# Optimization experiments

Measured on AMD Instinct MI355X. Metric: run time of the kernel, lower is better.

## Reference

```python
import jax, jax.numpy as jnp
import numpy as np

HIDDEN = 2048
HEADS = 16
HEAD_DIM = HIDDEN // HEADS          # 128
LATENT = HIDDEN // 4                # 512
ROPE_DIM = HEAD_DIM // 2            # 64 (dim passed to LlamaRotaryEmbedding)
B, S = 2, 2048
SCALE = 1.0 / np.sqrt(HEAD_DIM)


def _linear_params(key, d_in, d_out):
    kw, kb = jax.random.split(key)
    bound = 1.0 / np.sqrt(d_in)
    W = jax.random.uniform(kw, (d_in, d_out), jnp.float32, -bound, bound)
    b = jax.random.uniform(kb, (d_out,), jnp.float32, -bound, bound)
    return W, b


def _rope_tables(seq_len):
    # inv_freq over arange(0, ROPE_DIM, 2) -> ROPE_DIM//2 frequencies
    inv_freq = 1.0 / (10000.0 ** (np.arange(0, ROPE_DIM, 2, dtype=np.float32) / ROPE_DIM))
    t = np.arange(seq_len, dtype=np.float32)
    freqs = np.einsum('i,j->ij', t, inv_freq)  # [S, ROPE_DIM//2]
    return jnp.asarray(np.cos(freqs)), jnp.asarray(np.sin(freqs))


def setup_inputs() -> dict:
    key = jax.random.key(0)
    ks = jax.random.split(key, 10)
    x = jax.random.normal(ks[0], (B, S, HIDDEN), jnp.float32)
    # causal mask: 1 where attending allowed, 0 above the diagonal
    attention_mask = jnp.tril(jnp.ones((S, S), jnp.int32))[None].repeat(B, axis=0)
    W_kv_d, b_kv_d = _linear_params(ks[1], HIDDEN, LATENT)
    W_q_d, b_q_d = _linear_params(ks[2], HIDDEN, LATENT)
    W_k_u, b_k_u = _linear_params(ks[3], LATENT, HIDDEN // 2)
    W_q_u, b_q_u = _linear_params(ks[4], LATENT, HIDDEN // 2)
    W_v_u, b_v_u = _linear_params(ks[5], LATENT, HIDDEN)
    W_rk, b_rk = _linear_params(ks[6], HIDDEN, HIDDEN // 2)
    W_rq, b_rq = _linear_params(ks[7], LATENT, HIDDEN // 2)
    W_o, b_o = _linear_params(ks[8], HIDDEN, HIDDEN)
    return dict(x=x, attention_mask=attention_mask,
                W_kv_d=W_kv_d, b_kv_d=b_kv_d, W_q_d=W_q_d, b_q_d=b_q_d,
                W_k_u=W_k_u, b_k_u=b_k_u, W_q_u=W_q_u, b_q_u=b_q_u,
                W_v_u=W_v_u, b_v_u=b_v_u, W_rk=W_rk, b_rk=b_rk,
                W_rq=W_rq, b_rq=b_rq, W_o=W_o, b_o=b_o)


def _apply_rope(xr, cos, sin):
    # xr: [B,S,H,ROPE_DIM]; cos/sin: [S, ROPE_DIM//2]
    half = xr.shape[-1] // 2
    rot, pas = xr[..., :half], xr[..., half:]
    c = cos[None, :, None, :]
    s = sin[None, :, None, :]
    return jnp.concatenate([rot * c - pas * s, rot * s + pas * c], axis=-1)


def reference(x, attention_mask, W_kv_d, b_kv_d, W_q_d, b_q_d, W_k_u, b_k_u,
              W_q_u, b_q_u, W_v_u, b_v_u, W_rk, b_rk, W_rq, b_rq, W_o, b_o):
    Bsz, seq, _ = x.shape
    cos, sin = _rope_tables(seq)
    kv_d = x @ W_kv_d + b_kv_d                      # [B,S,latent]
    q_d = x @ W_q_d + b_q_d                         # [B,S,latent]
    k1 = (kv_d @ W_k_u + b_k_u).reshape(Bsz, seq, HEADS, HEAD_DIM // 2)
    q1 = (q_d @ W_q_u + b_q_u).reshape(Bsz, seq, HEADS, HEAD_DIM // 2)
    v = (kv_d @ W_v_u + b_v_u).reshape(Bsz, seq, HEADS, HEAD_DIM)
    k2 = (x @ W_rk + b_rk).reshape(Bsz, seq, HEADS, HEAD_DIM // 2)
    q2 = (q_d @ W_rq + b_rq).reshape(Bsz, seq, HEADS, HEAD_DIM // 2)
    k2 = _apply_rope(k2, cos, sin)
    q2 = _apply_rope(q2, cos, sin)
    k = jnp.concatenate([k1, k2], axis=-1)          # [B,S,H,head_dim]
    q = jnp.concatenate([q1, q2], axis=-1)
    scores = jnp.einsum('bqhd,bkhd->bhqk', q, k) * SCALE
    scores = jnp.where(attention_mask[:, None, :, :] == 0, -jnp.inf, scores)
    attn = jax.nn.softmax(scores, axis=-1)
    out = jnp.einsum('bhqk,bkhd->bqhd', attn, v).reshape(Bsz, seq, HIDDEN)
    return out @ W_o + b_o
```

## Files before the change

kernel.cpp:

```cpp
#include <hip/hip_runtime.h>
#include <hip/hip_bf16.h>
#include <math.h>

#define HIDDEN 2048
#define HEADS 16
#define HEAD_DIM 128
#define LATENT 512
#define SEQ 2048
#define BATCH 2
#define MROWS (BATCH*SEQ)
#define ATTN_SCALE 0.08838834764831845f

typedef unsigned short u16;
typedef __hip_bfloat16 bf16;
typedef __attribute__((ext_vector_type(8))) short bf16x8;
typedef __attribute__((ext_vector_type(4))) float f32x4;

__device__ inline float bf2f(u16 u) { return __uint_as_float(((unsigned)u) << 16); }
__device__ inline short f2bf_s(float v) { bf16 t = __float2bfloat16(v); return *(short*)&t; }

#define GLOAD_LDS(gp, lp) \
    __builtin_amdgcn_global_load_lds((const __attribute__((address_space(1))) unsigned int*)(gp), \
                                     (__attribute__((address_space(3))) unsigned int*)(lp), 16, 0, 0)

__global__ void rope_table_kernel(float* __restrict__ cosT, float* __restrict__ sinT) {
    int gid = blockIdx.x * blockDim.x + threadIdx.x;
    if (gid >= SEQ * 32) return;
    int t = gid >> 5, j = gid & 31;
    float inv = powf(10000.0f, -(float)j * (1.0f / 32.0f));
    float ang = (float)t * inv;
    cosT[gid] = cosf(ang);
    sinT[gid] = sinf(ang);
}

__global__ __launch_bounds__(256) void castx_kernel(const float* __restrict__ x, bf16* __restrict__ xb) {
    size_t gid = (size_t)blockIdx.x * 256 + threadIdx.x;
    const float* p = x + gid * 8;
    float4 a = *(const float4*)p;
    float4 b = *(const float4*)(p + 4);
    bf16 o[8] = {__float2bfloat16(a.x), __float2bfloat16(a.y), __float2bfloat16(a.z), __float2bfloat16(a.w),
                 __float2bfloat16(b.x), __float2bfloat16(b.y), __float2bfloat16(b.z), __float2bfloat16(b.w)};
    *(uint4*)(xb + gid * 8) = *(uint4*)o;
}

__global__ __launch_bounds__(256) void tcast_kernel(const float* __restrict__ W, bf16* __restrict__ Wt,
                                                    int K, int N) {
    __shared__ float T[32][33];
    int k0 = blockIdx.x * 32, n0 = blockIdx.y * 32;
    int tx = threadIdx.x & 31, ty = threadIdx.x >> 5;
#pragma unroll
    for (int p = 0; p < 4; p++) {
        int kr = p * 8 + ty;
        T[kr][tx] = W[(size_t)(k0 + kr) * N + n0 + tx];
    }
    __syncthreads();
#pragma unroll
    for (int p = 0; p < 4; p++) {
        int nr = p * 8 + ty;
        Wt[(size_t)(n0 + nr) * K + k0 + tx] = __float2bfloat16(T[tx][nr]);
    }
}

template<int FUSE>
__global__ __launch_bounds__(256) void mfma_gemm(
    const bf16* __restrict__ A, const bf16* __restrict__ Bt,
    const float* __restrict__ bias0, const float* __restrict__ bias1, const float* __restrict__ bias2,
    void* __restrict__ d0, void* __restrict__ d1, void* __restrict__ d2,
    const float* __restrict__ cosT, const float* __restrict__ sinT,
    int M, int N, int K)
{
    constexpr int BM = 128, BN = 128, BK = 32;
    __shared__ __align__(16) short As[2][BM * BK];
    __shared__ __align__(16) short Bs[2][BN * BK];

    const int tid = threadIdx.x;
    const int wid = tid >> 6;
    const int lane = tid & 63;
    const int wm = (wid >> 1) * 64;
    const int wn = (wid & 1) * 64;
    const int bm = blockIdx.y * BM, bn = blockIdx.x * BN;
    const int fr = lane & 15;
    const int fk = lane >> 4;

    const int srowA = wid * 32 + (lane >> 2);
    const int scol = (lane & 3) * 8;

    f32x4 acc[4][4];
#pragma unroll
    for (int mi = 0; mi < 4; mi++)
#pragma unroll
        for (int ni = 0; ni < 4; ni++)
            acc[mi][ni] = (f32x4){0.f, 0.f, 0.f, 0.f};

    const int NT = K / BK;
#pragma unroll
    for (int i = 0; i < 2; i++) {
        GLOAD_LDS(A + (size_t)(bm + srowA + i * 16) * K + scol, &As[0][(wid * 32 + i * 16) * BK]);
        GLOAD_LDS(Bt + (size_t)(bn + srowA + i * 16) * K + scol, &Bs[0][(wid * 32 + i * 16) * BK]);
    }

    int cur = 0;
    for (int t = 0; t < NT; t++) {
        __syncthreads();
        if (t + 1 < NT) {
            size_t kk = (size_t)(t + 1) * BK;
#pragma unroll
            for (int i = 0; i < 2; i++) {
                GLOAD_LDS(A + (size_t)(bm + srowA + i * 16) * K + kk + scol, &As[cur ^ 1][(wid * 32 + i * 16) * BK]);
                GLOAD_LDS(Bt + (size_t)(bn + srowA + i * 16) * K + kk + scol, &Bs[cur ^ 1][(wid * 32 + i * 16) * BK]);
            }
        }
        bf16x8 af[4], bfr[4];
#pragma unroll
        for (int mi = 0; mi < 4; mi++)
            af[mi] = *(const bf16x8*)&As[cur][(wm + mi * 16 + fr) * BK + fk * 8];
#pragma unroll
        for (int ni = 0; ni < 4; ni++)
            bfr[ni] = *(const bf16x8*)&Bs[cur][(wn + ni * 16 + fr) * BK + fk * 8];
#pragma unroll
        for (int mi = 0; mi < 4; mi++)
#pragma unroll
            for (int ni = 0; ni < 4; ni++)
                acc[mi][ni] = __builtin_amdgcn_mfma_f32_16x16x32_bf16(af[mi], bfr[ni], acc[mi][ni], 0, 0, 0);
        cur ^= 1;
    }

    const int cr = (lane >> 4) * 4;
#pragma unroll
    for (int mi = 0; mi < 4; mi++) {
#pragma unroll
        for (int j = 0; j < 4; j++) {
            int m = bm + wm + mi * 16 + cr + j;
            int bb = m >> 11;
            int s = m & 2047;

            if constexpr (FUSE == 4) {
#pragma unroll
                for (int ni = 0; ni < 4; ni++) {
                    int n = bn + wn + ni * 16 + fr;
                    ((float*)d0)[(size_t)m * N + n] = acc[mi][ni][j] + bias0[n];
                }
            } else if constexpr (FUSE == 1) {
                if (bn < 512) {
#pragma unroll
                    for (int ni = 0; ni < 4; ni++) {
                        int n = bn + wn + ni * 16 + fr;
                        ((bf16*)d0)[(size_t)m * 512 + n] = __float2bfloat16(acc[mi][ni][j] + bias0[n]);
                    }
                } else if (bn < 1024) {
#pragma unroll
                    for (int ni = 0; ni < 4; ni++) {
                        int n = bn + wn + ni * 16 + fr - 512;
                        ((bf16*)d1)[(size_t)m * 512 + n] = __float2bfloat16(acc[mi][ni][j] + bias1[n]);
                    }
                } else {
#pragma unroll
                    for (int ni = 0; ni < 2; ni++) {
                        int nl = bn + wn + ni * 16 + fr - 1024;
                        int hh = nl >> 6, dd = nl & 63;
                        float rot = acc[mi][ni][j] + bias2[nl];
                        float pas = acc[mi][ni + 2][j] + bias2[nl + 32];
                        float c = cosT[s * 32 + dd], sn = sinT[s * 32 + dd];
                        bf16* o = (bf16*)d2 + ((size_t)(bb * HEADS + hh) * SEQ + s) * HEAD_DIM + 64 + dd;
                        o[0]  = __float2bfloat16(rot * c - pas * sn);
                        o[32] = __float2bfloat16(rot * sn + pas * c);
                    }
                }
            } else if constexpr (FUSE == 2) {
                if (bn < 1024) {
#pragma unroll
                    for (int ni = 0; ni < 4; ni++) {
                        int nl = bn + wn + ni * 16 + fr;
                        int hh = nl >> 6, dd = nl & 63;
                        ((bf16*)d0)[((size_t)(bb * HEADS + hh) * SEQ + s) * HEAD_DIM + dd] =
                            __float2bfloat16(acc[mi][ni][j] + bias0[nl]);
                    }
                } else {
#pragma unroll
                    for (int ni = 0; ni < 4; ni++) {
                        int nl = bn + wn + ni * 16 + fr - 1024;
                        int hh = nl >> 7, dd = nl & 127;
                        ((bf16*)d1)[((size_t)(bb * HEADS + hh) * HEAD_DIM + dd) * SEQ + s] =
                            __float2bfloat16(acc[mi][ni][j] + bias1[nl]);
                    }
                }
            } else {
                if (bn < 1024) {
#pragma unroll
                    for (int ni = 0; ni < 4; ni++) {
                        int nl = bn + wn + ni * 16 + fr;
                        int hh = nl >> 6, dd = nl & 63;
                        ((bf16*)d0)[((size_t)(bb * HEADS + hh) * SEQ + s) * HEAD_DIM + dd] =
                            __float2bfloat16((acc[mi][ni][j] + bias0[nl]) * ATTN_SCALE);
                    }
                } else {
#pragma unroll
                    for (int ni = 0; ni < 2; ni++) {
                        int nl = bn + wn + ni * 16 + fr - 1024;
                        int hh = nl >> 6, dd = nl & 63;
                        float rot = (acc[mi][ni][j] + bias1[nl]) * ATTN_SCALE;
                        float pas = (acc[mi][ni + 2][j] + bias1[nl + 32]) * ATTN_SCALE;
                        float c = cosT[s * 32 + dd], sn = sinT[s * 32 + dd];
                        bf16* o = (bf16*)d1 + ((size_t)(bb * HEADS + hh) * SEQ + s) * HEAD_DIM + 64 + dd;
                        o[0]  = __float2bfloat16(rot * c - pas * sn);
                        o[32] = __float2bfloat16(rot * sn + pas * c);
                    }
                }
            }
        }
    }
}

__global__ __launch_bounds__(256) void attn_mfma_kernel(
    const bf16* __restrict__ qg, const bf16* __restrict__ kg,
    const bf16* __restrict__ vtg, bf16* __restrict__ outp)
{
    const int f = blockIdx.x;
    const int xcd = f & 7, slot = f >> 3;
    const int g = xcd * 4 + (slot >> 4);
    const int pid = slot & 15;
    const int b = g >> 4, h = g & 15;

    const int tid = threadIdx.x;
    const int w = tid >> 6, lane = tid & 63;
    const int fr = lane & 15, fq = lane >> 4;
    const int r7 = fr & 7;

    const bf16* Q  = qg  + (size_t)(b * HEADS + h) * SEQ * HEAD_DIM;
    const bf16* K  = kg  + (size_t)(b * HEADS + h) * SEQ * HEAD_DIM;
    const bf16* Vt = vtg + (size_t)(b * HEADS + h) * HEAD_DIM * SEQ;

    __shared__ __align__(16) short Ks[64 * 128];
    __shared__ __align__(16) short Vs[128 * 64];
    __shared__ __align__(16) short Ps[64 * 64];

#pragma unroll 1
    for (int seg = 0; seg < 2; seg++) {
        const int qt = seg ? (31 - pid) : pid;
        const int q0 = qt * 64;
        const int qrow = q0 + w * 16 + fr;

        bf16x8 qf[4];
#pragma unroll
        for (int kk = 0; kk < 4; kk++)
            qf[kk] = *(const bf16x8*)(Q + (size_t)(q0 + w * 16 + fr) * HEAD_DIM + kk * 32 + fq * 8);

        f32x4 accO[8];
#pragma unroll
        for (int ci = 0; ci < 8; ci++) accO[ci] = (f32x4){0.f, 0.f, 0.f, 0.f};
        float m_run = -INFINITY, l_run = 0.f;

        for (int kt = 0; kt <= qt; kt++) {
            __syncthreads();
#pragma unroll
            for (int p = 0; p < 4; p++) {
                int lin = tid + p * 256;
                int row = lin >> 4, ch = lin & 15;
                *(uint4*)&Ks[row * 128 + ((ch ^ (row & 7)) * 8)] =
                    *(const uint4*)(K + (size_t)(kt * 64 + row) * HEAD_DIM + ch * 8);
            }
#pragma unroll
            for (int p = 0; p < 4; p++) {
                int lin = tid + p * 256;
                int row = lin >> 3, ch = lin & 7;
                *(uint4*)&Vs[row * 64 + ((ch ^ (row & 7)) * 8)] =
                    *(const uint4*)(Vt + (size_t)row * SEQ + kt * 64 + ch * 8);
            }
            __syncthreads();

            f32x4 accS[4];
#pragma unroll
            for (int ni = 0; ni < 4; ni++) accS[ni] = (f32x4){0.f, 0.f, 0.f, 0.f};
#pragma unroll
            for (int kk = 0; kk < 4; kk++) {
#pragma unroll
                for (int ni = 0; ni < 4; ni++) {
                    bf16x8 kf = *(const bf16x8*)&Ks[(ni * 16 + fr) * 128 + (((kk * 4 + fq) ^ r7) * 8)];
                    accS[ni] = __builtin_amdgcn_mfma_f32_16x16x32_bf16(kf, qf[kk], accS[ni], 0, 0, 0);
                }
            }

            const bool diag = (kt == qt);
            float pv[16];
            float mloc = -INFINITY;
#pragma unroll
            for (int ni = 0; ni < 4; ni++)
#pragma unroll
                for (int reg = 0; reg < 4; reg++) {
                    float sc = accS[ni][reg];
                    int key = kt * 64 + ni * 16 + fq * 4 + reg;
                    if (diag && key > qrow) sc = -INFINITY;
                    pv[ni * 4 + reg] = sc;
                    mloc = fmaxf(mloc, sc);
                }
            mloc = fmaxf(mloc, __shfl_xor(mloc, 16));
            mloc = fmaxf(mloc, __shfl_xor(mloc, 32));
            float mn = fmaxf(m_run, mloc);
            float rs = __expf(m_run - mn);
            m_run = mn;
            float sum = 0.f;
#pragma unroll
            for (int i = 0; i < 16; i++) {
                float p = __expf(pv[i] - mn);
                pv[i] = p;
                sum += p;
            }
            sum += __shfl_xor(sum, 16);
            sum += __shfl_xor(sum, 32);
            l_run = l_run * rs + sum;

            if (__any(rs < 1.0f)) {
                float rsb[4];
#pragma unroll
                for (int reg = 0; reg < 4; reg++) rsb[reg] = __shfl(rs, fq * 4 + reg);
#pragma unroll
                for (int ci = 0; ci < 8; ci++)
#pragma unroll
                    for (int reg = 0; reg < 4; reg++)
                        accO[ci][reg] *= rsb[reg];
            }

#pragma unroll
            for (int ni = 0; ni < 4; ni++) {
                unsigned lo = (unsigned)(u16)f2bf_s(pv[ni * 4 + 0]) | ((unsigned)(u16)f2bf_s(pv[ni * 4 + 1]) << 16);
                unsigned hi = (unsigned)(u16)f2bf_s(pv[ni * 4 + 2]) | ((unsigned)(u16)f2bf_s(pv[ni * 4 + 3]) << 16);
                uint2 u; u.x = lo; u.y = hi;
                *(uint2*)&Ps[(w * 16 + fr) * 64 + (((2 * ni + (fq >> 1)) ^ r7) * 8) + (fq & 1) * 4] = u;
            }
            __syncthreads();

#pragma unroll
            for (int kk = 0; kk < 2; kk++) {
                bf16x8 pf = *(const bf16x8*)&Ps[(w * 16 + fr) * 64 + (((kk * 4 + fq) ^ r7) * 8)];
#pragma unroll
                for (int ci = 0; ci < 8; ci++) {
                    bf16x8 vf = *(const bf16x8*)&Vs[(ci * 16 + fr) * 64 + (((kk * 4 + fq) ^ r7) * 8)];
                    accO[ci] = __builtin_amdgcn_mfma_f32_16x16x32_bf16(pf, vf, accO[ci], 0, 0, 0);
                }
            }
        }

        float linv = 1.0f / l_run;
#pragma unroll
        for (int reg = 0; reg < 4; reg++) {
            float invb = __shfl(linv, fq * 4 + reg);
            bf16* dst = outp + ((size_t)(b * SEQ) + q0 + w * 16 + fq * 4 + reg) * HIDDEN + h * HEAD_DIM + fr;
#pragma unroll
            for (int ci = 0; ci < 8; ci++)
                dst[ci * 16] = __float2bfloat16(accO[ci][reg] * invb);
        }
    }
}

extern "C" void kernel_launch(void* const* d_in, const int* in_sizes, int n_in,
                              void* d_out, int out_size, void* d_ws, size_t ws_size,
                              hipStream_t stream)
{
    const float* x      = (const float*)d_in[0];
    const float* W_kv_d = (const float*)d_in[2];
    const float* b_kv_d = (const float*)d_in[3];
    const float* W_q_d  = (const float*)d_in[4];
    const float* b_q_d  = (const float*)d_in[5];
    const float* W_k_u  = (const float*)d_in[6];
    const float* b_k_u  = (const float*)d_in[7];
    const float* W_q_u  = (const float*)d_in[8];
    const float* b_q_u  = (const float*)d_in[9];
    const float* W_v_u  = (const float*)d_in[10];
    const float* b_v_u  = (const float*)d_in[11];
    const float* W_rk   = (const float*)d_in[12];
    const float* b_rk   = (const float*)d_in[13];
    const float* W_rq   = (const float*)d_in[14];
    const float* b_rq   = (const float*)d_in[15];
    const float* W_o    = (const float*)d_in[16];
    const float* b_o    = (const float*)d_in[17];

    float* cosT = (float*)d_ws;
    float* sinT = cosT + SEQ * 32;
    bf16* kv_d  = (bf16*)(sinT + SEQ * 32);
    bf16* q_d   = kv_d + (size_t)MROWS * LATENT;
    bf16* qg    = q_d + (size_t)MROWS * LATENT;
    bf16* kg    = qg + (size_t)BATCH * HEADS * SEQ * HEAD_DIM;
    bf16* vtg   = kg + (size_t)BATCH * HEADS * SEQ * HEAD_DIM;
    bf16* attnb = vtg + (size_t)BATCH * HEADS * SEQ * HEAD_DIM;
    bf16* xb    = attnb + (size_t)MROWS * HIDDEN;
    bf16* Wt_g1 = xb + (size_t)MROWS * HIDDEN;
    bf16* Wt_g2 = Wt_g1 + (size_t)2048 * HIDDEN;
    bf16* Wt_g3 = Wt_g2 + (size_t)3072 * LATENT;
    bf16* Wt_o  = Wt_g3 + (size_t)2048 * LATENT;

    rope_table_kernel<<<(SEQ * 32 + 255) / 256, 256, 0, stream>>>(cosT, sinT);
    castx_kernel<<<MROWS * HIDDEN / 8 / 256, 256, 0, stream>>>(x, xb);
    tcast_kernel<<<dim3(HIDDEN / 32, LATENT / 32), 256, 0, stream>>>(W_kv_d, Wt_g1, HIDDEN, LATENT);
    tcast_kernel<<<dim3(HIDDEN / 32, LATENT / 32), 256, 0, stream>>>(W_q_d, Wt_g1 + (size_t)512 * HIDDEN, HIDDEN, LATENT);
    tcast_kernel<<<dim3(HIDDEN / 32, 1024 / 32), 256, 0, stream>>>(W_rk, Wt_g1 + (size_t)1024 * HIDDEN, HIDDEN, 1024);
    tcast_kernel<<<dim3(LATENT / 32, 1024 / 32), 256, 0, stream>>>(W_k_u, Wt_g2, LATENT, 1024);
    tcast_kernel<<<dim3(LATENT / 32, HIDDEN / 32), 256, 0, stream>>>(W_v_u, Wt_g2 + (size_t)1024 * LATENT, LATENT, HIDDEN);
    tcast_kernel<<<dim3(LATENT / 32, 1024 / 32), 256, 0, stream>>>(W_q_u, Wt_g3, LATENT, 1024);
    tcast_kernel<<<dim3(LATENT / 32, 1024 / 32), 256, 0, stream>>>(W_rq, Wt_g3 + (size_t)1024 * LATENT, LATENT, 1024);
    tcast_kernel<<<dim3(HIDDEN / 32, HIDDEN / 32), 256, 0, stream>>>(W_o, Wt_o, HIDDEN, HIDDEN);

    mfma_gemm<1><<<dim3(2048 / 128, MROWS / 128), 256, 0, stream>>>(
        xb, Wt_g1, b_kv_d, b_q_d, b_rk, kv_d, q_d, kg, cosT, sinT, MROWS, 2048, HIDDEN);
    mfma_gemm<2><<<dim3(3072 / 128, MROWS / 128), 256, 0, stream>>>(
        kv_d, Wt_g2, b_k_u, b_v_u, nullptr, kg, vtg, nullptr, nullptr, nullptr, MROWS, 3072, LATENT);
    mfma_gemm<3><<<dim3(2048 / 128, MROWS / 128), 256, 0, stream>>>(
        q_d, Wt_g3, b_q_u, b_rq, nullptr, qg, qg, nullptr, cosT, sinT, MROWS, 2048, LATENT);

    attn_mfma_kernel<<<512, 256, 0, stream>>>(qg, kg, vtg, attnb);

    mfma_gemm<4><<<dim3(2048 / 128, MROWS / 128), 256, 0, stream>>>(
        attnb, Wt_o, b_o, nullptr, nullptr, d_out, nullptr, nullptr, nullptr, nullptr, MROWS, 2048, HIDDEN);
}
```

Measured before the change: 281.5 us.

## Double-buffer K/V tiles with async global-to-LDS prefetch in attention

The attention loop now keeps two LDS buffers for K and V. It uses direct global-to-LDS loads to prefetch the next key tile while the current one is being computed. The XOR swizzle moves from the LDS write address to the global read address, so each wave's LDS writes stay contiguous. The barrier between writing P and reading it is dropped, since each wave only touches its own P rows. This costs twice the K/V shared memory, which may lower occupancy, and correctness relies on the top-of-loop barrier waiting for the async loads to finish.

```diff
diff --git a/kernel.cpp b/kernel.cpp
--- a/kernel.cpp
+++ b/kernel.cpp
@@ -230,9 +230,14 @@
     const bf16* K  = kg  + (size_t)(b * HEADS + h) * SEQ * HEAD_DIM;
     const bf16* Vt = vtg + (size_t)(b * HEADS + h) * HEAD_DIM * SEQ;
 
-    __shared__ __align__(16) short Ks[64 * 128];
-    __shared__ __align__(16) short Vs[128 * 64];
+    __shared__ __align__(16) short Ks[2][64 * 128];
+    __shared__ __align__(16) short Vs[2][128 * 64];
     __shared__ __align__(16) short Ps[64 * 64];
+
+    const int krow = tid >> 4;
+    const int kch  = tid & 15;
+    const int vrow = tid >> 3;
+    const int vch  = tid & 7;
 
 #pragma unroll 1
     for (int seg = 0; seg < 2; seg++) {
@@ -250,23 +255,29 @@
         for (int ci = 0; ci < 8; ci++) accO[ci] = (f32x4){0.f, 0.f, 0.f, 0.f};
         float m_run = -INFINITY, l_run = 0.f;
 
+        __syncthreads();
+#pragma unroll
+        for (int p = 0; p < 4; p++) {
+            int rK = krow + p * 16;
+            GLOAD_LDS(K + (size_t)rK * HEAD_DIM + ((kch ^ (rK & 7)) * 8), &Ks[0][rK * 128 + kch * 8]);
+            int rV = vrow + p * 32;
+            GLOAD_LDS(Vt + (size_t)rV * SEQ + ((vch ^ (rV & 7)) * 8), &Vs[0][rV * 64 + vch * 8]);
+        }
+
+        int cur = 0;
         for (int kt = 0; kt <= qt; kt++) {
             __syncthreads();
-#pragma unroll
-            for (int p = 0; p < 4; p++) {
-                int lin = tid + p * 256;
-                int row = lin >> 4, ch = lin & 15;
-                *(uint4*)&Ks[row * 128 + ((ch ^ (row & 7)) * 8)] =
-                    *(const uint4*)(K + (size_t)(kt * 64 + row) * HEAD_DIM + ch * 8);
-            }
-#pragma unroll
-            for (int p = 0; p < 4; p++) {
-                int lin = tid + p * 256;
-                int row = lin >> 3, ch = lin & 7;
-                *(uint4*)&Vs[row * 64 + ((ch ^ (row & 7)) * 8)] =
-                    *(const uint4*)(Vt + (size_t)row * SEQ + kt * 64 + ch * 8);
-            }
-            __syncthreads();
+            if (kt < qt) {
+#pragma unroll
+                for (int p = 0; p < 4; p++) {
+                    int rK = krow + p * 16;
+                    GLOAD_LDS(K + (size_t)((kt + 1) * 64 + rK) * HEAD_DIM + ((kch ^ (rK & 7)) * 8),
+                              &Ks[cur ^ 1][rK * 128 + kch * 8]);
+                    int rV = vrow + p * 32;
+                    GLOAD_LDS(Vt + (size_t)rV * SEQ + (kt + 1) * 64 + ((vch ^ (rV & 7)) * 8),
+                              &Vs[cur ^ 1][rV * 64 + vch * 8]);
+                }
+            }
 
             f32x4 accS[4];
 #pragma unroll
@@ -275,7 +286,7 @@
             for (int kk = 0; kk < 4; kk++) {
 #pragma unroll
                 for (int ni = 0; ni < 4; ni++) {
-                    bf16x8 kf = *(const bf16x8*)&Ks[(ni * 16 + fr) * 128 + (((kk * 4 + fq) ^ r7) * 8)];
+                    bf16x8 kf = *(const bf16x8*)&Ks[cur][(ni * 16 + fr) * 128 + (((kk * 4 + fq) ^ r7) * 8)];
                     accS[ni] = __builtin_amdgcn_mfma_f32_16x16x32_bf16(kf, qf[kk], accS[ni], 0, 0, 0);
                 }
             }
@@ -327,17 +338,17 @@
                 uint2 u; u.x = lo; u.y = hi;
                 *(uint2*)&Ps[(w * 16 + fr) * 64 + (((2 * ni + (fq >> 1)) ^ r7) * 8) + (fq & 1) * 4] = u;
             }
-            __syncthreads();
 
 #pragma unroll
             for (int kk = 0; kk < 2; kk++) {
                 bf16x8 pf = *(const bf16x8*)&Ps[(w * 16 + fr) * 64 + (((kk * 4 + fq) ^ r7) * 8)];
 #pragma unroll
                 for (int ci = 0; ci < 8; ci++) {
-                    bf16x8 vf = *(const bf16x8*)&Vs[(ci * 16 + fr) * 64 + (((kk * 4 + fq) ^ r7) * 8)];
+                    bf16x8 vf = *(const bf16x8*)&Vs[cur][(ci * 16 + fr) * 64 + (((kk * 4 + fq) ^ r7) * 8)];
                     accO[ci] = __builtin_amdgcn_mfma_f32_16x16x32_bf16(pf, vf, accO[ci], 0, 0, 0);
                 }
             }
+            cur ^= 1;
         }
 
         float linv = 1.0f / l_run;
```

Result: faster. 271.8 us (-3.4%).
